# Kernel optimization log

Measured on AMD Instinct MI355X. Metric: run time of the kernel, lower is better.

## Reference

```python
import jax, jax.numpy as jnp
import numpy as np


def setup_inputs() -> dict:
    key = jax.random.key(0)
    ks = jax.random.split(key, 10)
    B, L, H, E, D = 2, 2048, 16, 64, 64
    d_model = 512
    inp = {
        "queries": jax.random.normal(ks[0], (B, L, H, E), jnp.float32),
        "keys": jax.random.normal(ks[1], (B, L, H, E), jnp.float32),
        "values": jax.random.normal(ks[2], (B, L, H, D), jnp.float32),
        "raw_series": jax.random.normal(ks[3], (B, L, d_model), jnp.float32),
        # learned fusion MLP: Linear(d_model, d_model//2) -> ReLU -> Linear(d_model//2, 1)
        "w1": jax.random.normal(ks[4], (d_model, d_model // 2), jnp.float32) / np.sqrt(d_model),
        "b1": jnp.zeros((d_model // 2,), jnp.float32),
        "w2": jax.random.normal(ks[5], (d_model // 2, 1), jnp.float32) / np.sqrt(d_model // 2),
        "b2": jnp.zeros((1,), jnp.float32),
        # per-head trend scaling, init ones
        "alpha_trend": jnp.ones((H,), jnp.float32),
    }
    return inp


MOMENTUM_ALPHA = 1.0
MOMENTUM_K = 1


def reference(queries, keys, values, raw_series, w1, b1, w2, b2, alpha_trend):
    B, L, H, E = queries.shape
    scale = 1.0 / jnp.sqrt(jnp.asarray(E, queries.dtype))

    # ---- soft momentum bias ----
    # learned fusion: MLP over features -> scalar per position, [B, L]
    h = jax.nn.relu(raw_series @ w1 + b1)
    fused = (h @ w2 + b2)[..., 0]                       # [B, L]
    k = max(1, min(MOMENTUM_K, L - 1))
    momentum = fused[:, k:] - fused[:, :-k]              # [B, L-k]
    momentum = jnp.pad(momentum, ((0, 0), (k, 0)))       # left-pad zeros -> [B, L]
    diff = jnp.abs(momentum[:, :, None] - momentum[:, None, :])  # [B, L, L]
    soft_bias = -MOMENTUM_ALPHA * diff                   # [B, L, L]

    # ---- attention ----
    scores = jnp.einsum('blhe,bshe->bhls', queries, keys)  # [B, H, L, L]
    scores = scores + soft_bias[:, None, :, :] * alpha_trend[None, :, None, None]
    causal = jnp.triu(jnp.ones((L, L), bool), k=1)       # True above diagonal
    scores = jnp.where(causal[None, None], -jnp.inf, scores)
    A = jax.nn.softmax(scale * scores, axis=-1)          # [B, H, L, L]
    V = jnp.einsum('bhls,bshd->blhd', A, values)         # [B, L, H, D]
    return V
```

## Files before the change

kernel.cpp:

```cpp
#include <hip/hip_runtime.h>
#include <math.h>

#define B_ 2
#define L_ 2048
#define H_ 16
#define E_ 64
#define D_ 64
#define DM_ 512
#define DH_ 256

typedef __bf16 bf16_t;
typedef bf16_t bf16x8_t __attribute__((ext_vector_type(8)));
typedef float f32x4_t __attribute__((ext_vector_type(4)));

__device__ __forceinline__ unsigned bpack(float hi, float lo) {
    unsigned uh = __float_as_uint(hi) + 0x8000u;
    unsigned ul = __float_as_uint(lo) + 0x8000u;
    return __builtin_amdgcn_perm(uh, ul, 0x07060302u);
}

__device__ __forceinline__ bf16_t to_bf16(float f) {
    union { float f; unsigned u; } x; x.f = f;
    unsigned r = (x.u + 0x7fffu + ((x.u >> 16) & 1u)) >> 16;
    union { unsigned short s; bf16_t b; } y; y.s = (unsigned short)r;
    return y.b;
}

__global__ __launch_bounds__(256) void transpose_w1_kernel(
        const float* __restrict__ w1, bf16_t* __restrict__ w1t) {
    const int n = blockIdx.x;
    const int t = threadIdx.x;
    #pragma unroll
    for (int u = 0; u < 2; ++u) {
        int k = t + u * 256;
        float v = w1[(size_t)k * DH_ + n];
        w1t[(size_t)n * DM_ + k] = to_bf16(v);
    }
}

__global__ __launch_bounds__(256) void mlp_kernel(
        const float* __restrict__ raw, const bf16_t* __restrict__ w1t,
        const float* __restrict__ b1, const float* __restrict__ w2,
        const float* __restrict__ b2, float* __restrict__ fused) {
    __shared__ bf16_t Rs[16][520];
    __shared__ float part[4][16];
    const int t = threadIdx.x;
    const int m0 = blockIdx.x * 16;
    #pragma unroll
    for (int u = 0; u < 8; ++u) {
        int idx = t + u * 256;
        int row = idx >> 7;
        int k = (idx & 127) << 2;
        f32x4_t v = *(const f32x4_t*)&raw[(size_t)(m0 + row) * DM_ + k];
        uint2 p;
        p.x = bpack(v[1], v[0]);
        p.y = bpack(v[3], v[2]);
        *(uint2*)&Rs[row][k] = p;
    }
    __syncthreads();
    const int wave = t >> 6;
    const int lane = t & 63;
    const int lrow = lane & 15;
    const int lgrp = lane >> 4;
    const int n0w = wave * 64;

    f32x4_t acc[4];
    #pragma unroll
    for (int nt = 0; nt < 4; ++nt) acc[nt] = (f32x4_t){0.f, 0.f, 0.f, 0.f};

    const bf16_t* wbase = w1t + (size_t)(n0w + lrow) * DM_ + lgrp * 8;
    #pragma unroll
    for (int s = 0; s < 16; ++s) {
        bf16x8_t a = *(const bf16x8_t*)&Rs[lrow][s * 32 + lgrp * 8];
        #pragma unroll
        for (int nt = 0; nt < 4; ++nt) {
            bf16x8_t b = *(const bf16x8_t*)(wbase + nt * 16 * DM_ + s * 32);
            acc[nt] = __builtin_amdgcn_mfma_f32_16x16x32_bf16(a, b, acc[nt], 0, 0, 0);
        }
    }
    float rowpart[4] = {0.f, 0.f, 0.f, 0.f};
    #pragma unroll
    for (int nt = 0; nt < 4; ++nt) {
        int n = n0w + nt * 16 + lrow;
        float b1v = b1[n];
        float w2v = w2[n];
        #pragma unroll
        for (int r = 0; r < 4; ++r) {
            float h = acc[nt][r] + b1v;
            h = h > 0.f ? h : 0.f;
            rowpart[r] += h * w2v;
        }
    }
    #pragma unroll
    for (int r = 0; r < 4; ++r) {
        float v = rowpart[r];
        v += __shfl_xor(v, 1);
        v += __shfl_xor(v, 2);
        v += __shfl_xor(v, 4);
        v += __shfl_xor(v, 8);
        if (lrow == 0) part[wave][lgrp * 4 + r] = v;
    }
    __syncthreads();
    if (t < 16)
        fused[m0 + t] = part[0][t] + part[1][t] + part[2][t] + part[3][t] + b2[0];
}

__global__ __launch_bounds__(256) void momentum_kernel(
        const float* __restrict__ fused, float* __restrict__ mom) {
    int i = blockIdx.x * 256 + threadIdx.x;
    if (i < B_ * L_) {
        int l = i & (L_ - 1);
        mom[i] = (l == 0) ? 0.f : fused[i] - fused[i - 1];
    }
}

struct TileRegs { f32x4_t k[4]; float v[16]; float m; };

__global__ __launch_bounds__(256) void attn_kernel(
        const float* __restrict__ Q, const float* __restrict__ K,
        const float* __restrict__ V, const float* __restrict__ mom,
        const float* __restrict__ alpha_trend, float* __restrict__ out) {
    __shared__ bf16_t Ks[64][72];
    __shared__ bf16_t Vt[64][72];
    __shared__ unsigned short Ps[4][16][68];
    __shared__ float moms[64];

    const int bid  = blockIdx.x;
    const int bh   = bid & 31;
    const int qt   = 31 - (bid >> 5);
    const int h    = bh & 15;
    const int b    = bh >> 4;
    const int q0   = qt << 6;
    const int tid  = threadIdx.x;
    const int wave = tid >> 6;
    const int lane = tid & 63;
    const int lrow = lane & 15;
    const int lgrp = lane >> 4;

    const float c1     = 0.18033688f;
    const float ascale2 = alpha_trend[h] * c1;
    const size_t bl    = (size_t)b * L_;
    const int qw0      = q0 + wave * 16;

    const float* Kb   = K + ((bl)*H_ + h) * E_;
    const float* Vb   = V + ((bl)*H_ + h) * D_;
    const float* momp = mom + bl;

    const int krow = tid >> 4;
    const int ke0  = (tid & 15) << 2;
    const int vd   = tid & 63;
    const int vsb  = tid >> 6;

    bf16x8_t a_lo, a_hi;
    {
        const float* qp = Q + ((bl + qw0 + lrow) * H_ + h) * E_ + lgrp * 8;
        f32x4_t v0 = *(const f32x4_t*)(qp);
        f32x4_t v1 = *(const f32x4_t*)(qp + 4);
        f32x4_t v2 = *(const f32x4_t*)(qp + 32);
        f32x4_t v3 = *(const f32x4_t*)(qp + 36);
        #pragma unroll
        for (int k = 0; k < 4; ++k) {
            a_lo[k]     = to_bf16(v0[k] * c1);
            a_lo[4 + k] = to_bf16(v1[k] * c1);
            a_hi[k]     = to_bf16(v2[k] * c1);
            a_hi[4 + k] = to_bf16(v3[k] * c1);
        }
    }
    float mq[4];
    #pragma unroll
    for (int r = 0; r < 4; ++r) mq[r] = momp[qw0 + lgrp * 4 + r];

    f32x4_t Oacc[4];
    #pragma unroll
    for (int c = 0; c < 4; ++c) Oacc[c] = (f32x4_t){0.f, 0.f, 0.f, 0.f};
    float rowsum[4] = {0.f, 0.f, 0.f, 0.f};

    TileRegs tr;
    {
        #pragma unroll
        for (int u = 0; u < 4; ++u)
            tr.k[u] = *(const f32x4_t*)&Kb[(krow + u * 16) * (H_ * E_) + ke0];
        #pragma unroll
        for (int j = 0; j < 16; ++j)
            tr.v[j] = Vb[(vsb * 16 + j) * (H_ * D_) + vd];
        tr.m = (tid < 64) ? momp[tid] : 0.f;
    }

    for (int st = 0; st <= qt; ++st) {
        __syncthreads();
        #pragma unroll
        for (int u = 0; u < 4; ++u) {
            uint2 p;
            p.x = bpack(tr.k[u][1], tr.k[u][0]);
            p.y = bpack(tr.k[u][3], tr.k[u][2]);
            *(uint2*)&Ks[krow + u * 16][ke0] = p;
        }
        #pragma unroll
        for (int u = 0; u < 4; ++u) {
            uint2 p;
            p.x = bpack(tr.v[u * 4 + 1], tr.v[u * 4 + 0]);
            p.y = bpack(tr.v[u * 4 + 3], tr.v[u * 4 + 2]);
            *(uint2*)&Vt[vd][vsb * 16 + u * 4] = p;
        }
        if (tid < 64) moms[tid] = tr.m;
        __syncthreads();

        if (st < qt) {
            const int s0n = (st + 1) << 6;
            #pragma unroll
            for (int u = 0; u < 4; ++u)
                tr.k[u] = *(const f32x4_t*)&Kb[(s0n + krow + u * 16) * (H_ * E_) + ke0];
            #pragma unroll
            for (int j = 0; j < 16; ++j)
                tr.v[j] = Vb[(s0n + vsb * 16 + j) * (H_ * D_) + vd];
            tr.m = (tid < 64) ? momp[s0n + tid] : 0.f;
        }

        f32x4_t Sacc[4];
        #pragma unroll
        for (int c = 0; c < 4; ++c) Sacc[c] = (f32x4_t){0.f, 0.f, 0.f, 0.f};
        #pragma unroll
        for (int c = 0; c < 4; ++c) {
            bf16x8_t b_lo = *(const bf16x8_t*)&Ks[c * 16 + lrow][lgrp * 8];
            bf16x8_t b_hi = *(const bf16x8_t*)&Ks[c * 16 + lrow][32 + lgrp * 8];
            Sacc[c] = __builtin_amdgcn_mfma_f32_16x16x32_bf16(a_lo, b_lo, Sacc[c], 0, 0, 0);
            Sacc[c] = __builtin_amdgcn_mfma_f32_16x16x32_bf16(a_hi, b_hi, Sacc[c], 0, 0, 0);
        }

        float rowe[4][4];
        #pragma unroll
        for (int c = 0; c < 4; ++c) {
            float ms = moms[c * 16 + lrow];
            #pragma unroll
            for (int r = 0; r < 4; ++r) {
                float arg = Sacc[c][r] - ascale2 * fabsf(mq[r] - ms);
                rowe[c][r] = __builtin_amdgcn_exp2f(arg);
            }
        }
        if (st == qt) {
            const int s0 = st << 6;
            #pragma unroll
            for (int c = 0; c < 4; ++c) {
                int sg = s0 + c * 16 + lrow;
                #pragma unroll
                for (int r = 0; r < 4; ++r)
                    if (sg > qw0 + lgrp * 4 + r) rowe[c][r] = 0.f;
            }
        }
        unsigned short* Psw = &Ps[wave][0][0];
        #pragma unroll
        for (int c = 0; c < 4; ++c) {
            #pragma unroll
            for (int r = 0; r < 4; ++r) {
                unsigned u = (__float_as_uint(rowe[c][r]) + 0x8000u) & 0xffff0000u;
                Psw[(lgrp * 4 + r) * 68 + c * 16 + lrow] = (unsigned short)(u >> 16);
                rowsum[r] += __uint_as_float(u);
            }
        }

        #pragma unroll
        for (int hh = 0; hh < 2; ++hh) {
            union { uint2 u2[2]; bf16x8_t v; } ab;
            ab.u2[0] = *(const uint2*)&Psw[lrow * 68 + hh * 32 + lgrp * 8];
            ab.u2[1] = *(const uint2*)&Psw[lrow * 68 + hh * 32 + lgrp * 8 + 4];
            #pragma unroll
            for (int c2 = 0; c2 < 4; ++c2) {
                bf16x8_t bv = *(const bf16x8_t*)&Vt[c2 * 16 + lrow][hh * 32 + lgrp * 8];
                Oacc[c2] = __builtin_amdgcn_mfma_f32_16x16x32_bf16(ab.v, bv, Oacc[c2], 0, 0, 0);
            }
        }
    }

    #pragma unroll
    for (int r = 0; r < 4; ++r) {
        float rs = rowsum[r];
        rs += __shfl_xor(rs, 1);
        rs += __shfl_xor(rs, 2);
        rs += __shfl_xor(rs, 4);
        rs += __shfl_xor(rs, 8);
        float inv = 1.f / rs;
        size_t orow = ((bl + qw0 + lgrp * 4 + r) * H_ + h) * D_;
        #pragma unroll
        for (int c = 0; c < 4; ++c)
            out[orow + c * 16 + lrow] = Oacc[c][r] * inv;
    }
}

extern "C" void kernel_launch(void* const* d_in, const int* in_sizes, int n_in,
                              void* d_out, int out_size, void* d_ws, size_t ws_size,
                              hipStream_t stream) {
    const float* Q     = (const float*)d_in[0];
    const float* K     = (const float*)d_in[1];
    const float* V     = (const float*)d_in[2];
    const float* raw   = (const float*)d_in[3];
    const float* w1    = (const float*)d_in[4];
    const float* b1    = (const float*)d_in[5];
    const float* w2    = (const float*)d_in[6];
    const float* b2    = (const float*)d_in[7];
    const float* alpha = (const float*)d_in[8];
    float* out = (float*)d_out;

    float* fused = (float*)d_ws;
    float* mom   = fused + B_ * L_;
    bf16_t* w1t  = (bf16_t*)(mom + B_ * L_);

    transpose_w1_kernel<<<DH_, 256, 0, stream>>>(w1, w1t);
    mlp_kernel<<<B_ * L_ / 16, 256, 0, stream>>>(raw, w1t, b1, w2, b2, fused);
    momentum_kernel<<<(B_ * L_ + 255) / 256, 256, 0, stream>>>(fused, mom);
    attn_kernel<<<B_ * H_ * (L_ / 64), 256, 0, stream>>>(Q, K, V, mom, alpha, out);
}
```

Before: 163.9 us.

## Keep P in registers via transposed QK^T MFMA, double-buffer K/V tiles

Computes S^T by swapping the MFMA operands and permuting K rows when staging them in LDS, so each lane's exponentiated scores already match the A-operand layout of the PV MFMA. This removes the per-wave P scratch in shared memory and its store/load round trip. The K/V/momentum tiles are double-buffered, which drops one barrier per iteration, and the transposed V tile uses an XOR swizzle to avoid bank conflicts. The rowsum now accumulates unrounded fp32 probabilities while P is bf16-rounded by bpack, a small numerical difference, and the double buffers increase LDS use.

```diff
diff --git a/kernel.cpp b/kernel.cpp
--- a/kernel.cpp
+++ b/kernel.cpp
@@ -120,10 +120,9 @@
         const float* __restrict__ Q, const float* __restrict__ K,
         const float* __restrict__ V, const float* __restrict__ mom,
         const float* __restrict__ alpha_trend, float* __restrict__ out) {
-    __shared__ bf16_t Ks[64][72];
-    __shared__ bf16_t Vt[64][72];
-    __shared__ unsigned short Ps[4][16][68];
-    __shared__ float moms[64];
+    __shared__ __align__(16) bf16_t Ks[2][64][72];
+    __shared__ __align__(16) bf16_t Vt[2][64][72];
+    __shared__ __align__(16) float moms[2][64];
 
     const int bid  = blockIdx.x;
     const int bh   = bid & 31;
@@ -137,17 +136,18 @@
     const int lrow = lane & 15;
     const int lgrp = lane >> 4;
 
-    const float c1     = 0.18033688f;
+    const float c1      = 0.18033688f;
     const float ascale2 = alpha_trend[h] * c1;
-    const size_t bl    = (size_t)b * L_;
-    const int qw0      = q0 + wave * 16;
-
-    const float* Kb   = K + ((bl)*H_ + h) * E_;
-    const float* Vb   = V + ((bl)*H_ + h) * D_;
+    const size_t bl     = (size_t)b * L_;
+    const int qw0       = q0 + wave * 16;
+
+    const float* Kb   = K + (bl * H_ + h) * E_;
+    const float* Vb   = V + (bl * H_ + h) * D_;
     const float* momp = mom + bl;
 
     const int krow = tid >> 4;
     const int ke0  = (tid & 15) << 2;
+    const int p0   = (krow & 3) | (((krow >> 3) & 1) << 2) | (((krow >> 2) & 1) << 4);
     const int vd   = tid & 63;
     const int vsb  = tid >> 6;
 
@@ -166,14 +166,12 @@
             a_hi[4 + k] = to_bf16(v3[k] * c1);
         }
     }
-    float mq[4];
-    #pragma unroll
-    for (int r = 0; r < 4; ++r) mq[r] = momp[qw0 + lgrp * 4 + r];
+    const float mq = momp[qw0 + lrow];
 
     f32x4_t Oacc[4];
     #pragma unroll
     for (int c = 0; c < 4; ++c) Oacc[c] = (f32x4_t){0.f, 0.f, 0.f, 0.f};
-    float rowsum[4] = {0.f, 0.f, 0.f, 0.f};
+    float rowsum = 0.f;
 
     TileRegs tr;
     {
@@ -186,23 +184,31 @@
         tr.m = (tid < 64) ? momp[tid] : 0.f;
     }
 
+    char* const vtbase = (char*)Vt;
+    const int vswz = ((vd >> 3) & 7) << 4;
+
     for (int st = 0; st <= qt; ++st) {
-        __syncthreads();
+        const int buf = st & 1;
+        bf16_t (*Ksb)[72] = Ks[buf];
+        char* vtb = vtbase + buf * (64 * 144);
+
         #pragma unroll
         for (int u = 0; u < 4; ++u) {
             uint2 p;
             p.x = bpack(tr.k[u][1], tr.k[u][0]);
             p.y = bpack(tr.k[u][3], tr.k[u][2]);
-            *(uint2*)&Ks[krow + u * 16][ke0] = p;
+            int pr = p0 + (u & 1) * 8 + (u >> 1) * 32;
+            *(uint2*)&Ksb[pr][ke0] = p;
         }
         #pragma unroll
         for (int u = 0; u < 4; ++u) {
             uint2 p;
             p.x = bpack(tr.v[u * 4 + 1], tr.v[u * 4 + 0]);
             p.y = bpack(tr.v[u * 4 + 3], tr.v[u * 4 + 2]);
-            *(uint2*)&Vt[vd][vsb * 16 + u * 4] = p;
-        }
-        if (tid < 64) moms[tid] = tr.m;
+            int boff = (vsb * 32 + u * 8) ^ vswz;
+            *(uint2*)(vtb + vd * 144 + boff) = p;
+        }
+        if (tid < 64) moms[buf][tid] = tr.m;
         __syncthreads();
 
         if (st < qt) {
@@ -221,64 +227,61 @@
         for (int c = 0; c < 4; ++c) Sacc[c] = (f32x4_t){0.f, 0.f, 0.f, 0.f};
         #pragma unroll
         for (int c = 0; c < 4; ++c) {
-            bf16x8_t b_lo = *(const bf16x8_t*)&Ks[c * 16 + lrow][lgrp * 8];
-            bf16x8_t b_hi = *(const bf16x8_t*)&Ks[c * 16 + lrow][32 + lgrp * 8];
-            Sacc[c] = __builtin_amdgcn_mfma_f32_16x16x32_bf16(a_lo, b_lo, Sacc[c], 0, 0, 0);
-            Sacc[c] = __builtin_amdgcn_mfma_f32_16x16x32_bf16(a_hi, b_hi, Sacc[c], 0, 0, 0);
+            bf16x8_t k_lo = *(const bf16x8_t*)&Ksb[c * 16 + lrow][lgrp * 8];
+            bf16x8_t k_hi = *(const bf16x8_t*)&Ksb[c * 16 + lrow][32 + lgrp * 8];
+            Sacc[c] = __builtin_amdgcn_mfma_f32_16x16x32_bf16(k_lo, a_lo, Sacc[c], 0, 0, 0);
+            Sacc[c] = __builtin_amdgcn_mfma_f32_16x16x32_bf16(k_hi, a_hi, Sacc[c], 0, 0, 0);
         }
 
         float rowe[4][4];
         #pragma unroll
         for (int c = 0; c < 4; ++c) {
-            float ms = moms[c * 16 + lrow];
+            const int sb = lgrp * 8 + ((c & 1) << 2) + ((c >> 1) << 5);
+            f32x4_t ms4 = *(const f32x4_t*)&moms[buf][sb];
             #pragma unroll
             for (int r = 0; r < 4; ++r) {
-                float arg = Sacc[c][r] - ascale2 * fabsf(mq[r] - ms);
+                float arg = Sacc[c][r] - ascale2 * fabsf(mq - ms4[r]);
                 rowe[c][r] = __builtin_amdgcn_exp2f(arg);
             }
         }
         if (st == qt) {
+            const int qg = qw0 + lrow;
             const int s0 = st << 6;
             #pragma unroll
             for (int c = 0; c < 4; ++c) {
-                int sg = s0 + c * 16 + lrow;
+                const int sg0 = s0 + lgrp * 8 + ((c & 1) << 2) + ((c >> 1) << 5);
                 #pragma unroll
                 for (int r = 0; r < 4; ++r)
-                    if (sg > qw0 + lgrp * 4 + r) rowe[c][r] = 0.f;
+                    if (sg0 + r > qg) rowe[c][r] = 0.f;
             }
         }
-        unsigned short* Psw = &Ps[wave][0][0];
-        #pragma unroll
-        for (int c = 0; c < 4; ++c) {
-            #pragma unroll
-            for (int r = 0; r < 4; ++r) {
-                unsigned u = (__float_as_uint(rowe[c][r]) + 0x8000u) & 0xffff0000u;
-                Psw[(lgrp * 4 + r) * 68 + c * 16 + lrow] = (unsigned short)(u >> 16);
-                rowsum[r] += __uint_as_float(u);
+        #pragma unroll
+        for (int c = 0; c < 4; ++c)
+            rowsum += (rowe[c][0] + rowe[c][1]) + (rowe[c][2] + rowe[c][3]);
+
+        #pragma unroll
+        for (int hh = 0; hh < 2; ++hh) {
+            union { unsigned u[4]; bf16x8_t v; } pa;
+            pa.u[0] = bpack(rowe[2 * hh][1],     rowe[2 * hh][0]);
+            pa.u[1] = bpack(rowe[2 * hh][3],     rowe[2 * hh][2]);
+            pa.u[2] = bpack(rowe[2 * hh + 1][1], rowe[2 * hh + 1][0]);
+            pa.u[3] = bpack(rowe[2 * hh + 1][3], rowe[2 * hh + 1][2]);
+            #pragma unroll
+            for (int c2 = 0; c2 < 4; ++c2) {
+                const int row = c2 * 16 + lrow;
+                int boff = (hh * 64 + lgrp * 16) ^ (((row >> 3) & 7) << 4);
+                bf16x8_t bv = *(const bf16x8_t*)(vtb + row * 144 + boff);
+                Oacc[c2] = __builtin_amdgcn_mfma_f32_16x16x32_bf16(pa.v, bv, Oacc[c2], 0, 0, 0);
             }
         }
-
-        #pragma unroll
-        for (int hh = 0; hh < 2; ++hh) {
-            union { uint2 u2[2]; bf16x8_t v; } ab;
-            ab.u2[0] = *(const uint2*)&Psw[lrow * 68 + hh * 32 + lgrp * 8];
-            ab.u2[1] = *(const uint2*)&Psw[lrow * 68 + hh * 32 + lgrp * 8 + 4];
-            #pragma unroll
-            for (int c2 = 0; c2 < 4; ++c2) {
-                bf16x8_t bv = *(const bf16x8_t*)&Vt[c2 * 16 + lrow][hh * 32 + lgrp * 8];
-                Oacc[c2] = __builtin_amdgcn_mfma_f32_16x16x32_bf16(ab.v, bv, Oacc[c2], 0, 0, 0);
-            }
-        }
-    }
-
+    }
+
+    float rs = rowsum;
+    rs += __shfl_xor(rs, 16);
+    rs += __shfl_xor(rs, 32);
     #pragma unroll
     for (int r = 0; r < 4; ++r) {
-        float rs = rowsum[r];
-        rs += __shfl_xor(rs, 1);
-        rs += __shfl_xor(rs, 2);
-        rs += __shfl_xor(rs, 4);
-        rs += __shfl_xor(rs, 8);
-        float inv = 1.f / rs;
+        float inv = 1.f / __shfl(rs, lgrp * 4 + r);
         size_t orow = ((bl + qw0 + lgrp * 4 + r) * H_ + h) * D_;
         #pragma unroll
         for (int c = 0; c < 4; ++c)
```

Result: no change. 162.3 us (-1.0%).
